# Kernel optimization log

Hardware: AMD Instinct MI355X
Metric: run time of the kernel (lower is better)

The kernel has to match this reference:

```python
import jax, jax.numpy as jnp
import numpy as np

D_M, L_OBS, ALPHA, D_H = 1024, 2048, 8192, 2048


def setup_inputs() -> dict:
    key = jax.random.key(0)
    k1, k2, k3, k4, k5 = jax.random.split(key, 5)
    x_ts = jax.random.normal(k1, (D_M, L_OBS), dtype=jnp.float32)
    t_ts = jax.random.randint(k2, (D_M, L_OBS), 0, ALPHA, dtype=jnp.int32)
    global_means = jax.random.normal(k3, (D_M,), dtype=jnp.float32)
    W = jax.random.normal(k4, (D_H, D_M), dtype=jnp.float32) * 0.02
    b = jax.random.normal(k5, (D_H,), dtype=jnp.float32) * 0.02
    return {"x_ts": x_ts, "t_ts": t_ts, "global_means": global_means, "W": W, "b": b}


def reference(x_ts, t_ts, global_means, W, b):
    d_m, l_obs = x_ts.shape
    alpha = ALPHA
    # valid observations: non-NaN value and time index within [0, alpha)
    valid = (~jnp.isnan(x_ts)) & (t_ts >= 0) & (t_ts < alpha)
    # route invalid observations to a dummy column `alpha` (dropped afterwards)
    idx = jnp.where(valid, t_ts, alpha)                      # [d_m, l_obs]
    rows = jnp.arange(d_m)[:, None]
    xs = jnp.where(valid, x_ts, 0.0)
    grid_val = jnp.zeros((d_m, alpha + 1), x_ts.dtype).at[rows, idx].set(xs)[:, :alpha]
    grid_ok = jnp.zeros((d_m, alpha + 1), bool).at[rows, idx].set(valid)[:, :alpha]
    # forward-fill: last valid index via cummax, init with global mean
    pos = jnp.arange(alpha)[None, :]                         # [1, alpha]
    last = jax.lax.cummax(jnp.where(grid_ok, pos, -1), axis=1)  # [d_m, alpha]
    filled = jnp.take_along_axis(grid_val, jnp.maximum(last, 0), axis=1)
    regular = jnp.where(last >= 0, filled, global_means[:, None])  # [d_m, alpha]
    # 1x1 conv over time == GEMM over feature dim; output [alpha, d_h]
    return jnp.einsum('ma,hm->ah', regular, W) + b[None, :]
```

## Files before the change

### kernel.cpp

```cpp
#include <hip/hip_runtime.h>
#include <stdint.h>

#define D_M   1024
#define L_OBS 2048
#define ALPHA 8192
#define D_H   2048

typedef __attribute__((ext_vector_type(8))) short short8;
typedef __attribute__((ext_vector_type(4))) float f32x4;

__device__ inline unsigned short f2bf(float f) {
  union { float f; unsigned u; } c; c.f = f;
  unsigned u = c.u;
  u += 0x7fffu + ((u >> 16) & 1u);
  return (unsigned short)(u >> 16);
}

__global__ __launch_bounds__(1024) void impute_fill(
    const float* __restrict__ x_ts, const int* __restrict__ t_ts,
    const float* __restrict__ gmean, unsigned short* __restrict__ dst,
    int transposed_out) {
  __shared__ unsigned long long pack[ALPHA];
  __shared__ float s_wv[16];
  __shared__ int   s_wh[16];

  const int m    = blockIdx.x;
  const int tid  = threadIdx.x;
  const int lane = tid & 63;
  const int wv   = tid >> 6;

  #pragma unroll
  for (int i = 0; i < 8; ++i) pack[tid + i * 1024] = 0ull;
  __syncthreads();

  #pragma unroll
  for (int j = 0; j < 2; ++j) {
    const int l = tid + j * 1024;
    const float xv = x_ts[(size_t)m * L_OBS + l];
    const int   tv = t_ts[(size_t)m * L_OBS + l];
    if ((xv == xv) && (tv >= 0) && (tv < ALPHA)) {
      union { float f; unsigned u; } c; c.f = xv;
      atomicMax(&pack[tv], ((unsigned long long)(l + 1) << 32) | c.u);
    }
  }
  __syncthreads();

  const int base = tid * 8;
  int has = 0; float lv = 0.f;
  #pragma unroll
  for (int i = 0; i < 8; ++i) {
    const unsigned long long p = pack[base + i];
    if (p >> 32) { has = 1; lv = __uint_as_float((unsigned)p); }
  }

  int ihas = has; float ilv = lv;
  #pragma unroll
  for (int d = 1; d < 64; d <<= 1) {
    const float pv = __shfl_up(ilv, d, 64);
    const int   ph = __shfl_up(ihas, d, 64);
    if (lane >= d && !ihas) { ihas = ph; ilv = pv; }
  }
  if (lane == 63) { s_wh[wv] = ihas; s_wv[wv] = ilv; }
  __syncthreads();
  if (wv == 0 && lane < 16) {
    int h2 = s_wh[lane]; float v2 = s_wv[lane];
    #pragma unroll
    for (int d = 1; d < 16; d <<= 1) {
      const float pv = __shfl_up(v2, d, 16);
      const int   ph = __shfl_up(h2, d, 16);
      if (lane >= d && !h2) { h2 = ph; v2 = pv; }
    }
    s_wh[lane] = h2; s_wv[lane] = v2;
  }
  __syncthreads();

  const float xlv = __shfl_up(ilv, 1, 64);
  const int   xh_ = __shfl_up(ihas, 1, 64);
  const int   xhas = (lane > 0) ? xh_ : 0;
  float running;
  if (xhas)                         running = xlv;
  else if (wv > 0 && s_wh[wv - 1])  running = s_wv[wv - 1];
  else                              running = gmean[m];

  if (transposed_out) {
    #pragma unroll
    for (int i = 0; i < 8; ++i) {
      const unsigned long long p = pack[base + i];
      if (p >> 32) running = __uint_as_float((unsigned)p);
      dst[(size_t)(base + i) * D_M + m] = f2bf(running);
    }
  } else {
    short8 ov;
    #pragma unroll
    for (int i = 0; i < 8; ++i) {
      const unsigned long long p = pack[base + i];
      if (p >> 32) running = __uint_as_float((unsigned)p);
      ov[i] = (short)f2bf(running);
    }
    *(short8*)&dst[(size_t)m * ALPHA + base] = ov;
  }
}

__global__ __launch_bounds__(256) void transpose_bf(
    const unsigned short* __restrict__ reg, unsigned short* __restrict__ regT) {
  __shared__ unsigned short tile[64 * 64];
  const int t  = threadIdx.x;
  const int m0 = (blockIdx.x & 15) * 64;
  const int A0 = (blockIdx.x >> 4) * 64;

  #pragma unroll
  for (int i = 0; i < 2; ++i) {
    const int m  = i * 32 + (t >> 3);
    const int ao = (t & 7) * 8;
    short8 v = *(const short8*)&reg[(size_t)(m0 + m) * ALPHA + A0 + ao];
    const int s = ((m & 7) ^ (m >> 3)) << 3;
    *(short8*)&tile[m * 64 + (ao ^ s)] = v;
  }
  __syncthreads();
  #pragma unroll
  for (int i = 0; i < 2; ++i) {
    const int a  = i * 32 + (t >> 3);
    const int mo = (t & 7) * 8;
    short8 ov;
    #pragma unroll
    for (int j = 0; j < 8; ++j) {
      const int mm = mo + j;
      const int s  = ((mm & 7) ^ (mm >> 3)) << 3;
      ov[j] = (short)tile[mm * 64 + (a ^ s)];
    }
    *(short8*)&regT[(size_t)(A0 + a) * D_M + m0 + mo] = ov;
  }
}

__global__ __launch_bounds__(256) void wconv(const float* __restrict__ W,
                                             unsigned short* __restrict__ Wb) {
  const int i = (blockIdx.x * 256 + threadIdx.x) * 4;
  const float4 w = *reinterpret_cast<const float4*>(&W[i]);
  ushort4 o;
  o.x = f2bf(w.x); o.y = f2bf(w.y); o.z = f2bf(w.z); o.w = f2bf(w.w);
  *reinterpret_cast<ushort4*>(&Wb[i]) = o;
}

#define GBM 256
#define GBN 256
#define GBK 32
#define GNT (D_M / GBK)

__device__ inline void gload_lds16(const void* g, void* l) {
  __builtin_amdgcn_global_load_lds(
      (const __attribute__((address_space(1))) unsigned int*)g,
      (__attribute__((address_space(3))) unsigned int*)l, 16, 0, 0);
}

#define BARX() { asm volatile("" ::: "memory"); __builtin_amdgcn_s_barrier(); \
                 asm volatile("" ::: "memory"); }

__global__ __launch_bounds__(512, 2) void gemm_bias(
    const unsigned short* __restrict__ A,
    const unsigned short* __restrict__ B,
    const float* __restrict__ bias, float* __restrict__ out) {
  __shared__ char lds[4 * 32768];

  const int tid  = threadIdx.x;
  const int lane = tid & 63;
  const int wid  = tid >> 6;
  const int wm   = wid >> 2;
  const int wn   = wid & 3;
  const int bn   = blockIdx.x & 7;
  const int bm   = blockIdx.x >> 3;
  const int a0 = bm * GBM, h0 = bn * GBN;

  f32x4 acc[8][4] = {};

  const int srow = tid >> 2;
  const int cbp  = ((tid & 3) * 16) ^ (((srow >> 1) & 3) << 4);
  const char* Abase = (const char*)A + ((size_t)(a0 + srow) * D_M) * 2 + cbp;
  const char* Bbase = (const char*)B + ((size_t)(h0 + srow) * D_M) * 2 + cbp;
  const size_t rstep = (size_t)128 * D_M * 2;

#define STAGE_A(kt) { const int s_ = ((kt) & 3) * 32768; const size_t ko_ = (size_t)(kt) * (GBK*2); \
  gload_lds16(Abase + ko_,         lds + s_ + tid * 16); \
  gload_lds16(Abase + ko_ + rstep, lds + s_ + 8192 + tid * 16); }
#define STAGE_B(kt) { const int s_ = ((kt) & 3) * 32768; const size_t ko_ = (size_t)(kt) * (GBK*2); \
  gload_lds16(Bbase + ko_,         lds + s_ + 16384 + tid * 16); \
  gload_lds16(Bbase + ko_ + rstep, lds + s_ + 16384 + 8192 + tid * 16); }

  const int rl   = lane & 15;
  const int kb   = (lane >> 4) * 16;
  const int rswz = ((rl >> 1) & 3) << 4;
  const int aoff = (wm * 128 + rl) * 64 + (kb ^ rswz);
  const int boff = 16384 + (wn * 64 + rl) * 64 + (kb ^ rswz);

  STAGE_A(0); STAGE_B(0); STAGE_A(1); STAGE_B(1); STAGE_A(2); STAGE_B(2);
  asm volatile("s_waitcnt vmcnt(8)" ::: "memory");
  BARX();

  #pragma unroll 4
  for (int kt = 0; kt < GNT; ++kt) {
    const int sb = (kt & 3) * 32768;
    short8 af[8], bf[4];
    #pragma unroll
    for (int n = 0; n < 4; ++n) bf[n] = *(const short8*)(lds + sb + boff + n * 1024);
    #pragma unroll
    for (int f = 0; f < 8; ++f) af[f] = *(const short8*)(lds + sb + aoff + f * 1024);
    if (kt < GNT - 3) { STAGE_A(kt + 3); STAGE_B(kt + 3); }
    __builtin_amdgcn_s_setprio(1);
    #pragma unroll
    for (int f = 0; f < 8; ++f)
      #pragma unroll
      for (int n = 0; n < 4; ++n)
        acc[f][n] = __builtin_amdgcn_mfma_f32_16x16x32_bf16(af[f], bf[n], acc[f][n], 0, 0, 0);
    __builtin_amdgcn_s_setprio(0);
    if (kt < GNT - 3)       { asm volatile("s_waitcnt vmcnt(8)" ::: "memory"); }
    else if (kt == GNT - 3) { asm volatile("s_waitcnt vmcnt(4)" ::: "memory"); }
    else if (kt == GNT - 2) { asm volatile("s_waitcnt vmcnt(0)" ::: "memory"); }
    BARX();
  }

  const int cl = lane & 15, rq = lane >> 4;
  #pragma unroll
  for (int n = 0; n < 4; ++n) {
    const int h = h0 + wn * 64 + n * 16 + cl;
    const float bv = bias[h];
    #pragma unroll
    for (int f = 0; f < 8; ++f) {
      const int ar = a0 + wm * 128 + f * 16 + rq * 4;
      #pragma unroll
      for (int r = 0; r < 4; ++r)
        out[(size_t)(ar + r) * D_H + h] = acc[f][n][r] + bv;
    }
  }
#undef STAGE_A
#undef STAGE_B
}

extern "C" void kernel_launch(void* const* d_in, const int* in_sizes, int n_in,
                              void* d_out, int out_size, void* d_ws, size_t ws_size,
                              hipStream_t stream) {
  const float* x  = (const float*)d_in[0];
  const int*   t  = (const int*)d_in[1];
  const float* gm = (const float*)d_in[2];
  const float* W  = (const float*)d_in[3];
  const float* b  = (const float*)d_in[4];
  float* out = (float*)d_out;

  const size_t SZ_REG = (size_t)ALPHA * D_M * 2;
  const size_t SZ_WB  = (size_t)D_H * D_M * 2;

  if (ws_size >= 2 * SZ_REG + SZ_WB) {
    unsigned short* reg  = (unsigned short*)d_ws;
    unsigned short* regT = (unsigned short*)((char*)d_ws + SZ_REG);
    unsigned short* Wb   = (unsigned short*)((char*)d_ws + 2 * SZ_REG);
    impute_fill<<<D_M, 1024, 0, stream>>>(x, t, gm, reg, 0);
    wconv<<<(D_H * D_M) / 1024, 256, 0, stream>>>(W, Wb);
    transpose_bf<<<(ALPHA / 64) * (D_M / 64), 256, 0, stream>>>(reg, regT);
    gemm_bias<<<(ALPHA / GBM) * (D_H / GBN), 512, 0, stream>>>(regT, Wb, b, out);
  } else {
    unsigned short* regT = (unsigned short*)d_ws;
    unsigned short* Wb   = (unsigned short*)((char*)d_ws + SZ_REG);
    impute_fill<<<D_M, 1024, 0, stream>>>(x, t, gm, regT, 1);
    wconv<<<(D_H * D_M) / 1024, 256, 0, stream>>>(W, Wb);
    gemm_bias<<<(ALPHA / GBM) * (D_H / GBN), 512, 0, stream>>>(regT, Wb, b, out);
  }
}
```

Before: 66.93 us.

## Restructure GEMM main loop into split A/B stages with phased MFMA ping-pong

Rewrites the bf16 GEMM mainloop so A and B tiles sit in separate 4-deep LDS ring buffers, each k-step is split into two MFMA phases over halves of the N fragments, and global-to-LDS loads for future steps are interleaved between phases. Barriers and explicit lgkmcnt/vmcnt waits bracket every phase, and the LDS swizzle pattern changes. The aim is to overlap LDS reads and global prefetch with MFMA work more finely and to reduce register pressure from B fragments. In exchange it adds twice as many barriers per k-step, and the hand-placed wait counts must stay correct.

```diff
diff --git a/kernel.cpp b/kernel.cpp
--- a/kernel.cpp
+++ b/kernel.cpp
@@ -141,10 +141,7 @@
   *reinterpret_cast<ushort4*>(&Wb[i]) = o;
 }
 
-#define GBM 256
-#define GBN 256
-#define GBK 32
-#define GNT (D_M / GBK)
+#define GNT 16
 
 __device__ inline void gload_lds16(const void* g, void* l) {
   __builtin_amdgcn_global_load_lds(
@@ -159,7 +156,7 @@
     const unsigned short* __restrict__ A,
     const unsigned short* __restrict__ B,
     const float* __restrict__ bias, float* __restrict__ out) {
-  __shared__ char lds[4 * 32768];
+  __shared__ char lds[131072];
 
   const int tid  = threadIdx.x;
   const int lane = tid & 63;
@@ -168,53 +165,92 @@
   const int wn   = wid & 3;
   const int bn   = blockIdx.x & 7;
   const int bm   = blockIdx.x >> 3;
-  const int a0 = bm * GBM, h0 = bn * GBN;
+  const int a0 = bm * 256, h0 = bn * 256;
 
   f32x4 acc[8][4] = {};
-
-  const int srow = tid >> 2;
-  const int cbp  = ((tid & 3) * 16) ^ (((srow >> 1) & 3) << 4);
-  const char* Abase = (const char*)A + ((size_t)(a0 + srow) * D_M) * 2 + cbp;
-  const char* Bbase = (const char*)B + ((size_t)(h0 + srow) * D_M) * 2 + cbp;
-  const size_t rstep = (size_t)128 * D_M * 2;
-
-#define STAGE_A(kt) { const int s_ = ((kt) & 3) * 32768; const size_t ko_ = (size_t)(kt) * (GBK*2); \
-  gload_lds16(Abase + ko_,         lds + s_ + tid * 16); \
-  gload_lds16(Abase + ko_ + rstep, lds + s_ + 8192 + tid * 16); }
-#define STAGE_B(kt) { const int s_ = ((kt) & 3) * 32768; const size_t ko_ = (size_t)(kt) * (GBK*2); \
-  gload_lds16(Bbase + ko_,         lds + s_ + 16384 + tid * 16); \
-  gload_lds16(Bbase + ko_ + rstep, lds + s_ + 16384 + 8192 + tid * 16); }
-
-  const int rl   = lane & 15;
-  const int kb   = (lane >> 4) * 16;
-  const int rswz = ((rl >> 1) & 3) << 4;
-  const int aoff = (wm * 128 + rl) * 64 + (kb ^ rswz);
-  const int boff = 16384 + (wn * 64 + rl) * 64 + (kb ^ rswz);
-
-  STAGE_A(0); STAGE_B(0); STAGE_A(1); STAGE_B(1); STAGE_A(2); STAGE_B(2);
-  asm volatile("s_waitcnt vmcnt(8)" ::: "memory");
+  short8 af[8], bf[2];
+
+  const int r0 = tid >> 2, s0 = tid & 3;
+  const int swzB = ((s0 ^ (r0 & 3)) * 16);
+  const char* Asrc0 = (const char*)A + ((size_t)(a0 + r0) * D_M) * 2 + swzB;
+  const char* Asrc1 = Asrc0 + (size_t)128 * D_M * 2;
+  const char* Bsrc0 = (const char*)B + ((size_t)(h0 + r0) * D_M) * 2 + swzB;
+  const char* Bsrc1 = Bsrc0 + (size_t)128 * D_M * 2;
+
+#define STAGE_A(kh) { char* d_ = lds + ((kh) & 3) * 16384 + tid * 16; \
+  gload_lds16(Asrc0 + (size_t)(kh) * 64, d_); \
+  gload_lds16(Asrc1 + (size_t)(kh) * 64, d_ + 8192); }
+#define STAGE_B(kh) { char* d_ = lds + 65536 + ((kh) & 3) * 16384 + tid * 16; \
+  gload_lds16(Bsrc0 + (size_t)(kh) * 64, d_); \
+  gload_lds16(Bsrc1 + (size_t)(kh) * 64, d_ + 8192); }
+
+  const int rl  = lane & 15;
+  const int rsw = ((lane >> 4) ^ (lane & 3)) * 16;
+  const int Aro = (wm * 128 + rl) * 64 + rsw;
+  const int Bro = 65536 + (wn * 64 + rl) * 64 + rsw;
+
+#define RD_A(kh) { _Pragma("unroll") \
+  for (int mf = 0; mf < 8; ++mf) \
+    af[mf] = *(const short8*)(lds + ((kh) & 3) * 16384 + Aro + mf * 1024); }
+#define RD_B(kh, np) { \
+  bf[0] = *(const short8*)(lds + ((kh) & 3) * 16384 + Bro + ((np) * 2 + 0) * 1024); \
+  bf[1] = *(const short8*)(lds + ((kh) & 3) * 16384 + Bro + ((np) * 2 + 1) * 1024); }
+
+#define PH_MFMA(NP) \
+  BARX(); \
+  asm volatile("s_waitcnt lgkmcnt(0)" ::: "memory"); \
+  __builtin_amdgcn_sched_barrier(0); \
+  __builtin_amdgcn_s_setprio(1); \
+  _Pragma("unroll") \
+  for (int mf = 0; mf < 8; ++mf) { \
+    acc[mf][(NP)*2+0] = __builtin_amdgcn_mfma_f32_16x16x32_bf16(af[mf], bf[0], acc[mf][(NP)*2+0], 0, 0, 0); \
+    acc[mf][(NP)*2+1] = __builtin_amdgcn_mfma_f32_16x16x32_bf16(af[mf], bf[1], acc[mf][(NP)*2+1], 0, 0, 0); \
+  } \
+  __builtin_amdgcn_s_setprio(0); \
   BARX();
 
-  #pragma unroll 4
-  for (int kt = 0; kt < GNT; ++kt) {
-    const int sb = (kt & 3) * 32768;
-    short8 af[8], bf[4];
-    #pragma unroll
-    for (int n = 0; n < 4; ++n) bf[n] = *(const short8*)(lds + sb + boff + n * 1024);
-    #pragma unroll
-    for (int f = 0; f < 8; ++f) af[f] = *(const short8*)(lds + sb + aoff + f * 1024);
-    if (kt < GNT - 3) { STAGE_A(kt + 3); STAGE_B(kt + 3); }
-    __builtin_amdgcn_s_setprio(1);
-    #pragma unroll
-    for (int f = 0; f < 8; ++f)
-      #pragma unroll
-      for (int n = 0; n < 4; ++n)
-        acc[f][n] = __builtin_amdgcn_mfma_f32_16x16x32_bf16(af[f], bf[n], acc[f][n], 0, 0, 0);
-    __builtin_amdgcn_s_setprio(0);
-    if (kt < GNT - 3)       { asm volatile("s_waitcnt vmcnt(8)" ::: "memory"); }
-    else if (kt == GNT - 3) { asm volatile("s_waitcnt vmcnt(4)" ::: "memory"); }
-    else if (kt == GNT - 2) { asm volatile("s_waitcnt vmcnt(0)" ::: "memory"); }
-    BARX();
+  STAGE_A(0); STAGE_B(0); STAGE_A(1); STAGE_B(1); STAGE_A(2); STAGE_B(2); STAGE_A(3);
+  asm volatile("s_waitcnt vmcnt(6)" ::: "memory");
+  BARX();
+
+  for (int t = 0; t < GNT - 2; ++t) {
+    const int kh0 = 2 * t, kh1 = 2 * t + 1;
+    RD_A(kh0); RD_B(kh0, 0);
+    STAGE_B(kh0 + 3);
+    PH_MFMA(0);
+    RD_B(kh0, 1);
+    STAGE_A(kh0 + 4);
+    PH_MFMA(1);
+    RD_A(kh1); RD_B(kh1, 0);
+    STAGE_B(kh0 + 4);
+    PH_MFMA(0);
+    RD_B(kh1, 1);
+    STAGE_A(kh0 + 5);
+    asm volatile("s_waitcnt vmcnt(6)" ::: "memory");
+    PH_MFMA(1);
+  }
+  {
+    RD_A(28); RD_B(28, 0);
+    STAGE_B(31);
+    PH_MFMA(0);
+    RD_B(28, 1);
+    PH_MFMA(1);
+    RD_A(29); RD_B(29, 0);
+    PH_MFMA(0);
+    RD_B(29, 1);
+    asm volatile("s_waitcnt vmcnt(4)" ::: "memory");
+    PH_MFMA(1);
+  }
+  {
+    RD_A(30); RD_B(30, 0);
+    PH_MFMA(0);
+    RD_B(30, 1);
+    asm volatile("s_waitcnt vmcnt(0)" ::: "memory");
+    PH_MFMA(1);
+    RD_A(31); RD_B(31, 0);
+    PH_MFMA(0);
+    RD_B(31, 1);
+    PH_MFMA(1);
   }
 
   const int cl = lane & 15, rq = lane >> 4;
@@ -232,6 +268,9 @@
   }
 #undef STAGE_A
 #undef STAGE_B
+#undef RD_A
+#undef RD_B
+#undef PH_MFMA
 }
 
 extern "C" void kernel_launch(void* const* d_in, const int* in_sizes, int n_in,
@@ -254,12 +293,12 @@
     impute_fill<<<D_M, 1024, 0, stream>>>(x, t, gm, reg, 0);
     wconv<<<(D_H * D_M) / 1024, 256, 0, stream>>>(W, Wb);
     transpose_bf<<<(ALPHA / 64) * (D_M / 64), 256, 0, stream>>>(reg, regT);
-    gemm_bias<<<(ALPHA / GBM) * (D_H / GBN), 512, 0, stream>>>(regT, Wb, b, out);
+    gemm_bias<<<(ALPHA / 256) * (D_H / 256), 512, 0, stream>>>(regT, Wb, b, out);
   } else {
     unsigned short* regT = (unsigned short*)d_ws;
     unsigned short* Wb   = (unsigned short*)((char*)d_ws + SZ_REG);
     impute_fill<<<D_M, 1024, 0, stream>>>(x, t, gm, regT, 1);
     wconv<<<(D_H * D_M) / 1024, 256, 0, stream>>>(W, Wb);
-    gemm_bias<<<(ALPHA / GBM) * (D_H / GBN), 512, 0, stream>>>(regT, Wb, b, out);
-  }
-}
+    gemm_bias<<<(ALPHA / 256) * (D_H / 256), 512, 0, stream>>>(regT, Wb, b, out);
+  }
+}
```

After: 69.87 us. 4.4% more time.

## Shrink GEMM block tile to 128x256 with 3-stage LDS ring for higher occupancy

Applied to the files above, without the earlier changes.

The bf16 GEMM block tile shrinks from 256x256 to 128x256, and the 4-stage LDS ring buffer (128KB) becomes a 3-stage one (72KB). Launch bounds go from 2 to 4 waves-per-EU so more blocks can be resident and the grid doubles. The main loop is manually unrolled by three with an explicit lgkmcnt wait and a sched_barrier before the MFMA burst. The goal is better latency hiding through occupancy and a grid that fills the CUs more evenly. The cost is less operand reuse per block (more A/B refetch from L2) and a shallower prefetch depth.

```diff
diff --git a/kernel.cpp b/kernel.cpp
--- a/kernel.cpp
+++ b/kernel.cpp
@@ -141,10 +141,7 @@
   *reinterpret_cast<ushort4*>(&Wb[i]) = o;
 }
 
-#define GBM 256
-#define GBN 256
-#define GBK 32
-#define GNT (D_M / GBK)
+#define GNT3 32
 
 __device__ inline void gload_lds16(const void* g, void* l) {
   __builtin_amdgcn_global_load_lds(
@@ -154,12 +151,14 @@
 
 #define BARX() { asm volatile("" ::: "memory"); __builtin_amdgcn_s_barrier(); \
                  asm volatile("" ::: "memory"); }
-
-__global__ __launch_bounds__(512, 2) void gemm_bias(
+#define LGKM0() asm volatile("s_waitcnt lgkmcnt(0)" ::: "memory")
+#define SB0()   __builtin_amdgcn_sched_barrier(0)
+
+__global__ __launch_bounds__(512, 4) void gemm_bias(
     const unsigned short* __restrict__ A,
     const unsigned short* __restrict__ B,
     const float* __restrict__ bias, float* __restrict__ out) {
-  __shared__ char lds[4 * 32768];
+  __shared__ char lds[73728];
 
   const int tid  = threadIdx.x;
   const int lane = tid & 63;
@@ -168,70 +167,75 @@
   const int wn   = wid & 3;
   const int bn   = blockIdx.x & 7;
   const int bm   = blockIdx.x >> 3;
-  const int a0 = bm * GBM, h0 = bn * GBN;
-
-  f32x4 acc[8][4] = {};
-
-  const int srow = tid >> 2;
-  const int cbp  = ((tid & 3) * 16) ^ (((srow >> 1) & 3) << 4);
-  const char* Abase = (const char*)A + ((size_t)(a0 + srow) * D_M) * 2 + cbp;
-  const char* Bbase = (const char*)B + ((size_t)(h0 + srow) * D_M) * 2 + cbp;
-  const size_t rstep = (size_t)128 * D_M * 2;
-
-#define STAGE_A(kt) { const int s_ = ((kt) & 3) * 32768; const size_t ko_ = (size_t)(kt) * (GBK*2); \
-  gload_lds16(Abase + ko_,         lds + s_ + tid * 16); \
-  gload_lds16(Abase + ko_ + rstep, lds + s_ + 8192 + tid * 16); }
-#define STAGE_B(kt) { const int s_ = ((kt) & 3) * 32768; const size_t ko_ = (size_t)(kt) * (GBK*2); \
-  gload_lds16(Bbase + ko_,         lds + s_ + 16384 + tid * 16); \
-  gload_lds16(Bbase + ko_ + rstep, lds + s_ + 16384 + 8192 + tid * 16); }
-
-  const int rl   = lane & 15;
-  const int kb   = (lane >> 4) * 16;
-  const int rswz = ((rl >> 1) & 3) << 4;
-  const int aoff = (wm * 128 + rl) * 64 + (kb ^ rswz);
-  const int boff = 16384 + (wn * 64 + rl) * 64 + (kb ^ rswz);
-
-  STAGE_A(0); STAGE_B(0); STAGE_A(1); STAGE_B(1); STAGE_A(2); STAGE_B(2);
-  asm volatile("s_waitcnt vmcnt(8)" ::: "memory");
+  const int a0r = bm * 128, h0 = bn * 256;
+
+  f32x4 acc[4][4] = {};
+  short8 af[4], bf[4];
+
+  const int r0 = tid >> 2, s0 = tid & 3;
+  const int swzB = (s0 ^ ((r0 >> 1) & 3)) * 16;
+  const char* Asrc  = (const char*)A + ((size_t)(a0r + r0) * D_M) * 2 + swzB;
+  const char* Bsrc0 = (const char*)B + ((size_t)(h0 + r0) * D_M) * 2 + swzB;
+  const char* Bsrc1 = Bsrc0 + (size_t)128 * D_M * 2;
+
+#define STAGE(S, kt) { \
+  gload_lds16(Asrc  + (size_t)(kt) * 64, lds + (S) * 8192 + tid * 16); \
+  char* bd_ = lds + 24576 + (S) * 16384 + tid * 16; \
+  gload_lds16(Bsrc0 + (size_t)(kt) * 64, bd_); \
+  gload_lds16(Bsrc1 + (size_t)(kt) * 64, bd_ + 8192); }
+
+  const int rl  = lane & 15;
+  const int rsw = (((lane >> 4) ^ ((rl >> 1) & 3))) * 16;
+  const int Aro = (wm * 64 + rl) * 64 + rsw;
+  const int Bro = 24576 + (wn * 64 + rl) * 64 + rsw;
+
+#define TILE(S, SST, T) { \
+  _Pragma("unroll") \
+  for (int mf = 0; mf < 4; ++mf) \
+    af[mf] = *(const short8*)(lds + (S) * 8192 + Aro + mf * 1024); \
+  _Pragma("unroll") \
+  for (int nf = 0; nf < 4; ++nf) \
+    bf[nf] = *(const short8*)(lds + (S) * 16384 + Bro + nf * 1024); \
+  if ((T) < GNT3 - 2) STAGE(SST, (T) + 2); \
+  LGKM0(); SB0(); \
+  __builtin_amdgcn_s_setprio(1); \
+  _Pragma("unroll") \
+  for (int mf = 0; mf < 4; ++mf) \
+    _Pragma("unroll") \
+    for (int nf = 0; nf < 4; ++nf) \
+      acc[mf][nf] = __builtin_amdgcn_mfma_f32_16x16x32_bf16(af[mf], bf[nf], acc[mf][nf], 0, 0, 0); \
+  __builtin_amdgcn_s_setprio(0); \
+  if ((T) < GNT3 - 2)       { asm volatile("s_waitcnt vmcnt(3)" ::: "memory"); } \
+  else if ((T) == GNT3 - 2) { asm volatile("s_waitcnt vmcnt(0)" ::: "memory"); } \
+  if ((T) < GNT3 - 1) BARX(); }
+
+  STAGE(0, 0); STAGE(1, 1);
+  asm volatile("s_waitcnt vmcnt(3)" ::: "memory");
   BARX();
 
-  #pragma unroll 4
-  for (int kt = 0; kt < GNT; ++kt) {
-    const int sb = (kt & 3) * 32768;
-    short8 af[8], bf[4];
-    #pragma unroll
-    for (int n = 0; n < 4; ++n) bf[n] = *(const short8*)(lds + sb + boff + n * 1024);
-    #pragma unroll
-    for (int f = 0; f < 8; ++f) af[f] = *(const short8*)(lds + sb + aoff + f * 1024);
-    if (kt < GNT - 3) { STAGE_A(kt + 3); STAGE_B(kt + 3); }
-    __builtin_amdgcn_s_setprio(1);
-    #pragma unroll
-    for (int f = 0; f < 8; ++f)
-      #pragma unroll
-      for (int n = 0; n < 4; ++n)
-        acc[f][n] = __builtin_amdgcn_mfma_f32_16x16x32_bf16(af[f], bf[n], acc[f][n], 0, 0, 0);
-    __builtin_amdgcn_s_setprio(0);
-    if (kt < GNT - 3)       { asm volatile("s_waitcnt vmcnt(8)" ::: "memory"); }
-    else if (kt == GNT - 3) { asm volatile("s_waitcnt vmcnt(4)" ::: "memory"); }
-    else if (kt == GNT - 2) { asm volatile("s_waitcnt vmcnt(0)" ::: "memory"); }
-    BARX();
-  }
+  for (int tt = 0; tt < GNT3 - 2; tt += 3) {
+    TILE(0, 2, tt);
+    TILE(1, 0, tt + 1);
+    TILE(2, 1, tt + 2);
+  }
+  TILE(0, 2, 30);
+  TILE(1, 0, 31);
 
   const int cl = lane & 15, rq = lane >> 4;
   #pragma unroll
-  for (int n = 0; n < 4; ++n) {
-    const int h = h0 + wn * 64 + n * 16 + cl;
+  for (int nf = 0; nf < 4; ++nf) {
+    const int h = h0 + wn * 64 + nf * 16 + cl;
     const float bv = bias[h];
     #pragma unroll
-    for (int f = 0; f < 8; ++f) {
-      const int ar = a0 + wm * 128 + f * 16 + rq * 4;
+    for (int mf = 0; mf < 4; ++mf) {
+      const int ar = a0r + wm * 64 + mf * 16 + rq * 4;
       #pragma unroll
       for (int r = 0; r < 4; ++r)
-        out[(size_t)(ar + r) * D_H + h] = acc[f][n][r] + bv;
-    }
-  }
-#undef STAGE_A
-#undef STAGE_B
+        out[(size_t)(ar + r) * D_H + h] = acc[mf][nf][r] + bv;
+    }
+  }
+#undef STAGE
+#undef TILE
 }
 
 extern "C" void kernel_launch(void* const* d_in, const int* in_sizes, int n_in,
@@ -254,12 +258,12 @@
     impute_fill<<<D_M, 1024, 0, stream>>>(x, t, gm, reg, 0);
     wconv<<<(D_H * D_M) / 1024, 256, 0, stream>>>(W, Wb);
     transpose_bf<<<(ALPHA / 64) * (D_M / 64), 256, 0, stream>>>(reg, regT);
-    gemm_bias<<<(ALPHA / GBM) * (D_H / GBN), 512, 0, stream>>>(regT, Wb, b, out);
+    gemm_bias<<<(ALPHA / 128) * (D_H / 256), 512, 0, stream>>>(regT, Wb, b, out);
   } else {
     unsigned short* regT = (unsigned short*)d_ws;
     unsigned short* Wb   = (unsigned short*)((char*)d_ws + SZ_REG);
     impute_fill<<<D_M, 1024, 0, stream>>>(x, t, gm, regT, 1);
     wconv<<<(D_H * D_M) / 1024, 256, 0, stream>>>(W, Wb);
-    gemm_bias<<<(ALPHA / GBM) * (D_H / GBN), 512, 0, stream>>>(regT, Wb, b, out);
-  }
-}
+    gemm_bias<<<(ALPHA / 128) * (D_H / 256), 512, 0, stream>>>(regT, Wb, b, out);
+  }
+}
```

Result: no change. 67.87 us (+1.4%).
